# Kernel optimization log

Hardware: AMD Instinct MI355X
Metric: run time of the kernel (lower is better)

Reference implementation:

```python
import jax, jax.numpy as jnp
import numpy as np
from jax import lax

NALGOS = 64
NTASKS = 1024
LX_LEN = 512
TASK_DIFFICULTY_SCALE = 1.0


def setup_inputs() -> dict:
    key = jax.random.key(0)
    k1, k2, k3, k4, k5, k6 = jax.random.split(key, 6)
    lx = jax.random.randint(k1, (LX_LEN,), 0, NTASKS)
    # task similarity in [-1, 1] as in the original (np.random.random * 2 - 1)
    task_matrix = jax.random.uniform(k2, (NTASKS, NTASKS), dtype=jnp.float32) * 2.0 - 1.0
    # difficulty in (0, 1); offset slightly away from 0 for numerical sanity of result/difficulty
    task_difficulty = jax.random.uniform(k3, (NTASKS,), dtype=jnp.float32, minval=0.05, maxval=1.0)
    alg_efficiency = 0.5 + 0.02 * jax.random.normal(k4, (NALGOS,), dtype=jnp.float32)
    alg_memory = 0.5 + 0.10 * jax.random.normal(k5, (NALGOS,), dtype=jnp.float32)
    alg_experience_boost = 0.5 + 0.02 * jax.random.normal(k6, (NALGOS,), dtype=jnp.float32)
    return {
        "lx": lx,
        "task_matrix": task_matrix,
        "task_difficulty": task_difficulty,
        "alg_efficiency": alg_efficiency,
        "alg_memory": alg_memory,
        "alg_experience_boost": alg_experience_boost,
    }


def _performance(lx, task_matrix, task_difficulty, alg_efficiency, alg_memory, alg_experience_boost):
    nalgos = alg_efficiency.shape[0]
    ntasks = task_matrix.shape[0]
    dtype = task_matrix.dtype
    diff = task_difficulty * TASK_DIFFICULTY_SCALE  # [T]

    eff = alg_efficiency[:, None]          # [A,1]
    mem = alg_memory[:, None]              # [A,1]
    boost = alg_experience_boost[:, None]  # [A,1]

    def step(carry, task):
        result, sig = carry                 # each [A,T]
        row = task_matrix[task]             # [T] similarity of current lx task to every task2
        prior_perf = sig[:, task][:, None]  # [A,1] sig of current lx task at previous step
        result_next = result * mem + row[None, :] * (eff + prior_perf * boost)
        sig_next = jax.nn.sigmoid(result_next / diff[None, :]) * 2.0 - 1.0
        return (result_next, sig_next), sig_next

    init = (jnp.zeros((nalgos, ntasks), dtype), jnp.zeros((nalgos, ntasks), dtype))
    _, sig_steps = lax.scan(step, init, lx)  # [L,A,T]
    sig_steps = jnp.transpose(sig_steps, (1, 2, 0))  # [A,T,L]
    # prepend the zero initial step -> [A,T,L+1], matching torch output layout
    zero0 = jnp.zeros((nalgos, ntasks, 1), dtype)
    return jnp.concatenate([zero0, sig_steps], axis=-1)


def reference(lx, task_matrix, task_difficulty, alg_efficiency, alg_memory, alg_experience_boost):
    return _performance(lx, task_matrix, task_difficulty, alg_efficiency, alg_memory, alg_experience_boost)
```

## Files before the change

kernel.cpp:

```cpp
#include <hip/hip_runtime.h>

#define NALGOS 64
#define NTASKS 1024
#define LXLEN  512
#define TOUT   (LXLEN + 1)
#define PROWS  (LXLEN + 8)

__device__ __forceinline__ float rdlane(float v, int lane) {
    return __int_as_float(__builtin_amdgcn_readlane(__float_as_int(v), lane));
}

__global__ __launch_bounds__(256) void phase0_kernel(
    const int* __restrict__ lx, const float* __restrict__ tm,
    float* __restrict__ P)
{
    const int t = blockIdx.x;
    const int i = threadIdx.x;
    if (t < LXLEN) {
        const int row = lx[t] * NTASKS;
        P[t * LXLEN + i]       = tm[row + lx[i]];
        P[t * LXLEN + i + 256] = tm[row + lx[i + 256]];
    } else {
        P[t * LXLEN + i]       = 0.f;
        P[t * LXLEN + i + 256] = 0.f;
    }
}

__global__ __launch_bounds__(64) void phase1_kernel(
    const int*   __restrict__ lx,
    const float* __restrict__ P,
    const float* __restrict__ diff,
    const float* __restrict__ eff_g,
    const float* __restrict__ mem_g,
    const float* __restrict__ boost_g,
    float*       __restrict__ coef_out)
{
    const int a = blockIdx.x, lane = threadIdx.x;

    float nk[8]; float V[8];
    #pragma unroll
    for (int k = 0; k < 8; ++k) {
        const int tsk = lx[lane + 64 * k];
        nk[k] = -1.4426950408889634f / diff[tsk];
        V[k] = 0.f;
    }
    const float eff = eff_g[a], mem = mem_g[a], boost = boost_g[a];

    float G[8][8];
    #pragma unroll
    for (int d = 0; d < 8; ++d)
        #pragma unroll
        for (int k = 0; k < 8; ++k)
            G[d][k] = P[d * LXLEN + 64 * k + lane];

    float coef = eff;
    float* cout = coef_out + (size_t)a * LXLEN;

    #pragma unroll
    for (int q = 0; q < 8; ++q) {
        float cbuf = 0.f;
        for (int g = 0; g < 8; ++g) {
            const int tb = q * 64 + g * 8;
            #pragma unroll
            for (int j = 0; j < 8; ++j) {
                const float p = V[q] * nk[q];
                float x = rdlane(p, g * 8 + j);
                x = fminf(fmaxf(x, -126.f), 126.f);
                const float e = __builtin_exp2f(x);
                const float u = (1.f - e) * __builtin_amdgcn_rcpf(1.f + e);
                coef = __builtin_fmaf(u, boost, eff);
                cbuf = (lane == g * 8 + j) ? coef : cbuf;
                #pragma unroll
                for (int k = q; k < 8; ++k)
                    V[k] = __builtin_fmaf(V[k], mem, G[j][k] * coef);
                const float* rp = P + (tb + j + 8) * LXLEN + lane;
                #pragma unroll
                for (int k = q; k < 8; ++k)
                    G[j][k] = rp[64 * k];
            }
        }
        cout[q * 64 + lane] = cbuf;
    }
}

__global__ __launch_bounds__(256, 4) void phase2_kernel(
    const int*   __restrict__ lx,
    const float* __restrict__ tm,
    const float* __restrict__ diff,
    const float* __restrict__ mem_g,
    const float* __restrict__ coef,
    float*       __restrict__ out)
{
    const int b   = blockIdx.x;
    const int a   = b >> 5;
    const int c   = (b >> 2) & 7;
    const int seg = b & 3;
    const int tid = threadIdx.x;
    const int n   = (seg << 8) | tid;

    const int warm = (c >= 2) ? 128 : 64 * c;
    const int t0   = 64 * c - 1 - warm;

    __shared__ __align__(16) int   task_sh[224];
    __shared__ __align__(16) float coef_sh[224];
    __shared__ __align__(16) float ring[32 * 257];

    const int nfill = warm + 96;
    for (int i = tid; i < nfill; i += 256) {
        const int t = t0 + i;
        const bool ok = (t >= 0) && (t < LXLEN);
        task_sh[i] = ok ? lx[t] : 0;
        coef_sh[i] = ok ? coef[a * LXLEN + t] : 0.f;
    }

    const float mem   = mem_g[a];
    const float negkd = -1.4426950408889634f / diff[n];
    const int   d     = (16 - (n & 15)) & 15;
    float* rowp = out + ((size_t)a * NTASKS + n) * TOUT;
    float  r    = 0.f;
    float* ringc = ring + tid;

    const int wb = tid & 192;
    const int lq = tid & 15;
    const int qq = (tid >> 4) & 3;

    __syncthreads();

    float rbuf[16];
    #pragma unroll
    for (int j = 0; j < 16; ++j) {
        const int tk = __builtin_amdgcn_readfirstlane(task_sh[j]);
        rbuf[j] = tm[(size_t)tk * NTASKS + n];
    }

    for (int base = 0; base < warm; base += 16) {
        float nbuf[16];
        #pragma unroll
        for (int j = 0; j < 16; ++j) {
            const int tk = __builtin_amdgcn_readfirstlane(task_sh[base + 16 + j]);
            nbuf[j] = tm[(size_t)tk * NTASKS + n];
        }
        #pragma unroll
        for (int v = 0; v < 4; ++v) {
            const float4 cq = *(const float4*)&coef_sh[base + 4 * v];
            r = __builtin_fmaf(r, mem, rbuf[4 * v + 0] * cq.x);
            r = __builtin_fmaf(r, mem, rbuf[4 * v + 1] * cq.y);
            r = __builtin_fmaf(r, mem, rbuf[4 * v + 2] * cq.z);
            r = __builtin_fmaf(r, mem, rbuf[4 * v + 3] * cq.w);
        }
        #pragma unroll
        for (int j = 0; j < 16; ++j) rbuf[j] = nbuf[j];
    }

    #pragma unroll
    for (int rr = 0; rr < 5; ++rr) {
        const int base = warm + 16 * rr;
        float nbuf[16];
        #pragma unroll
        for (int j = 0; j < 16; ++j) {
            const int tk = __builtin_amdgcn_readfirstlane(task_sh[base + 16 + j]);
            nbuf[j] = tm[(size_t)tk * NTASKS + n];
        }
        #pragma unroll
        for (int v = 0; v < 4; ++v) {
            const float4 cq = *(const float4*)&coef_sh[base + 4 * v];
            const float cf[4] = { cq.x, cq.y, cq.z, cq.w };
            #pragma unroll
            for (int u4 = 0; u4 < 4; ++u4) {
                const int j = 4 * v + u4;
                r = __builtin_fmaf(r, mem, rbuf[j] * cf[u4]);
                float x = r * negkd;
                x = fminf(fmaxf(x, -126.f), 126.f);
                const float e = __builtin_exp2f(x);
                const float sig = (1.f - e) * __builtin_amdgcn_rcpf(1.f + e);
                ringc[((16 * rr + j - d) & 31) * 257] = sig;
                if (c == 0 && rr == 0 && j < d) rowp[j] = sig;
            }
        }
        if (rr >= 1) {
            const int g    = rr - 1;
            const int sb16 = (g & 1) << 4;
            #pragma unroll
            for (int sub = 0; sub < 16; ++sub) {
                const int tau = wb + 4 * sub + qq;
                const int nn  = (seg << 8) | tau;
                const int dd  = (16 - qq - 4 * (sub & 3)) & 15;
                const float vv = ring[(sb16 + lq) * 257 + tau];
                if (!(c == 7 && g == 3 && dd > 1)) {
                    out[((size_t)a * NTASKS + nn) * TOUT
                        + 64 * c + dd + 16 * g + lq] = vv;
                }
            }
        }
        #pragma unroll
        for (int j = 0; j < 16; ++j) rbuf[j] = nbuf[j];
    }

    if (c == 7) {
        const int tt0 = (d == 1) ? 513 : ((d == 0) ? 512 : 496 + d);
        #pragma unroll
        for (int u = 496; u <= 512; ++u) {
            if (u >= tt0) rowp[u] = ringc[(((u - 448) - d) & 31) * 257];
        }
    }
}

__global__ __launch_bounds__(1024) void fused_fallback_kernel(
    const int* __restrict__ lx, const float* __restrict__ tm,
    const float* __restrict__ diff, const float* __restrict__ eff_g,
    const float* __restrict__ mem_g, const float* __restrict__ boost_g,
    float* __restrict__ out)
{
    const int a = blockIdx.x, n = threadIdx.x;
    __shared__ int lx_sh[LXLEN];
    __shared__ float sbuf[2];
    if (n < LXLEN) lx_sh[n] = lx[n];
    if (n == 0) sbuf[0] = 0.0f;
    const float eff = eff_g[a], mem = mem_g[a], boost = boost_g[a];
    const float negkd = -1.4426950408889634f / diff[n];
    float* outp = out + ((size_t)a * NTASKS + n) * TOUT;
    outp[0] = 0.0f;
    float r = 0.0f;
    __syncthreads();
    for (int t = 0; t < LXLEN; ++t) {
        const int task = lx_sh[t];
        const float s = sbuf[t & 1];
        const float coef = __builtin_fmaf(s, boost, eff);
        const float row = tm[task * NTASKS + n];
        r = __builtin_fmaf(r, mem, row * coef);
        float x = r * negkd;
        x = fminf(fmaxf(x, -126.0f), 126.0f);
        const float e = __builtin_exp2f(x);
        const float sig = (1.0f - e) * __builtin_amdgcn_rcpf(1.0f + e);
        outp[t + 1] = sig;
        if (t + 1 < LXLEN && n == lx_sh[t + 1]) sbuf[(t + 1) & 1] = sig;
        __syncthreads();
    }
}

extern "C" void kernel_launch(void* const* d_in, const int* in_sizes, int n_in,
                              void* d_out, int out_size, void* d_ws, size_t ws_size,
                              hipStream_t stream) {
    const int*   lx    = (const int*)  d_in[0];
    const float* tm    = (const float*)d_in[1];
    const float* diff  = (const float*)d_in[2];
    const float* eff   = (const float*)d_in[3];
    const float* mem   = (const float*)d_in[4];
    const float* boost = (const float*)d_in[5];
    float* out = (float*)d_out;

    const size_t coef_elems = (size_t)NALGOS * LXLEN;
    const size_t P_elems    = (size_t)PROWS * LXLEN;
    const size_t need_bytes = (coef_elems + P_elems) * sizeof(float);

    if (ws_size >= need_bytes) {
        float* coef = (float*)d_ws;
        float* P    = coef + coef_elems;
        phase0_kernel<<<dim3(PROWS), dim3(256), 0, stream>>>(lx, tm, P);
        phase1_kernel<<<dim3(NALGOS), dim3(64), 0, stream>>>(
            lx, P, diff, eff, mem, boost, coef);
        phase2_kernel<<<dim3(NALGOS * 32), dim3(256), 0, stream>>>(
            lx, tm, diff, mem, coef, out);
    } else {
        fused_fallback_kernel<<<dim3(NALGOS), dim3(NTASKS), 0, stream>>>(
            lx, tm, diff, eff, mem, boost, out);
    }
}
```

Baseline: 225.9 us.

## Process eight algorithms per phase2 thread to reuse task_matrix loads

Phase2 blocks now handle 8 algorithms at once with 128-thread blocks, so each gathered task_matrix value is reused across 8 recurrences instead of being reloaded once per algorithm. The transpose ring buffer is reorganized per algorithm with a 16-row layout, and the tail write-out is folded into the main loop. Phase1 simplifies the sigmoid-to-coefficient formula into a single rcp plus fma and drops the exp clamp. The changes cut global gather traffic but raise register pressure and shrink the grid to 512 blocks, which may lower occupancy.

```diff
diff --git a/kernel.cpp b/kernel.cpp
--- a/kernel.cpp
+++ b/kernel.cpp
@@ -45,6 +45,7 @@
         V[k] = 0.f;
     }
     const float eff = eff_g[a], mem = mem_g[a], boost = boost_g[a];
+    const float twob = 2.f * boost, effmb = eff - boost;
 
     float G[8][8];
     #pragma unroll
@@ -64,11 +65,10 @@
             #pragma unroll
             for (int j = 0; j < 8; ++j) {
                 const float p = V[q] * nk[q];
-                float x = rdlane(p, g * 8 + j);
-                x = fminf(fmaxf(x, -126.f), 126.f);
+                const float x = rdlane(p, g * 8 + j);
                 const float e = __builtin_exp2f(x);
-                const float u = (1.f - e) * __builtin_amdgcn_rcpf(1.f + e);
-                coef = __builtin_fmaf(u, boost, eff);
+                const float w = __builtin_amdgcn_rcpf(1.f + e);
+                coef = __builtin_fmaf(twob, w, effmb);
                 cbuf = (lane == g * 8 + j) ? coef : cbuf;
                 #pragma unroll
                 for (int k = q; k < 8; ++k)
@@ -83,7 +83,7 @@
     }
 }
 
-__global__ __launch_bounds__(256, 4) void phase2_kernel(
+__global__ __launch_bounds__(128, 2) void phase2_kernel(
     const int*   __restrict__ lx,
     const float* __restrict__ tm,
     const float* __restrict__ diff,
@@ -92,35 +92,41 @@
     float*       __restrict__ out)
 {
     const int b   = blockIdx.x;
-    const int a   = b >> 5;
-    const int c   = (b >> 2) & 7;
-    const int seg = b & 3;
+    const int ag  = b >> 6;
+    const int c   = (b >> 3) & 7;
+    const int seg = b & 7;
     const int tid = threadIdx.x;
-    const int n   = (seg << 8) | tid;
-
-    const int warm = (c >= 2) ? 128 : 64 * c;
-    const int t0   = 64 * c - 1 - warm;
+    const int n   = (seg << 7) | tid;
+
+    const int warm  = (c >= 2) ? 128 : 64 * c;
+    const int t0    = 64 * c - 1 - warm;
+    const int nfill = warm + 96;
 
     __shared__ __align__(16) int   task_sh[224];
-    __shared__ __align__(16) float coef_sh[224];
-    __shared__ __align__(16) float ring[32 * 257];
-
-    const int nfill = warm + 96;
-    for (int i = tid; i < nfill; i += 256) {
+    __shared__ __align__(16) float coef_sh[8][224];
+    __shared__ __align__(16) float ring[8][16][129];
+
+    for (int i = tid; i < nfill; i += 128) {
         const int t = t0 + i;
         const bool ok = (t >= 0) && (t < LXLEN);
         task_sh[i] = ok ? lx[t] : 0;
-        coef_sh[i] = ok ? coef[a * LXLEN + t] : 0.f;
-    }
-
-    const float mem   = mem_g[a];
+        #pragma unroll
+        for (int g = 0; g < 8; ++g)
+            coef_sh[g][i] = ok ? coef[(ag * 8 + g) * LXLEN + t] : 0.f;
+    }
+
+    float memv[8];
+    #pragma unroll
+    for (int g = 0; g < 8; ++g) memv[g] = mem_g[ag * 8 + g];
+
     const float negkd = -1.4426950408889634f / diff[n];
     const int   d     = (16 - (n & 15)) & 15;
-    float* rowp = out + ((size_t)a * NTASKS + n) * TOUT;
-    float  r    = 0.f;
-    float* ringc = ring + tid;
-
-    const int wb = tid & 192;
+
+    float r[8];
+    #pragma unroll
+    for (int g = 0; g < 8; ++g) r[g] = 0.f;
+
+    const int wb = tid & 64;
     const int lq = tid & 15;
     const int qq = (tid >> 4) & 3;
 
@@ -142,17 +148,20 @@
         }
         #pragma unroll
         for (int v = 0; v < 4; ++v) {
-            const float4 cq = *(const float4*)&coef_sh[base + 4 * v];
-            r = __builtin_fmaf(r, mem, rbuf[4 * v + 0] * cq.x);
-            r = __builtin_fmaf(r, mem, rbuf[4 * v + 1] * cq.y);
-            r = __builtin_fmaf(r, mem, rbuf[4 * v + 2] * cq.z);
-            r = __builtin_fmaf(r, mem, rbuf[4 * v + 3] * cq.w);
+            #pragma unroll
+            for (int g = 0; g < 8; ++g) {
+                const float4 cq = *(const float4*)&coef_sh[g][base + 4 * v];
+                const float mg = memv[g];
+                r[g] = __builtin_fmaf(r[g], mg, rbuf[4 * v + 0] * cq.x);
+                r[g] = __builtin_fmaf(r[g], mg, rbuf[4 * v + 1] * cq.y);
+                r[g] = __builtin_fmaf(r[g], mg, rbuf[4 * v + 2] * cq.z);
+                r[g] = __builtin_fmaf(r[g], mg, rbuf[4 * v + 3] * cq.w);
+            }
         }
         #pragma unroll
         for (int j = 0; j < 16; ++j) rbuf[j] = nbuf[j];
     }
 
-    #pragma unroll
     for (int rr = 0; rr < 5; ++rr) {
         const int base = warm + 16 * rr;
         float nbuf[16];
@@ -162,46 +171,58 @@
             nbuf[j] = tm[(size_t)tk * NTASKS + n];
         }
         #pragma unroll
-        for (int v = 0; v < 4; ++v) {
-            const float4 cq = *(const float4*)&coef_sh[base + 4 * v];
-            const float cf[4] = { cq.x, cq.y, cq.z, cq.w };
-            #pragma unroll
-            for (int u4 = 0; u4 < 4; ++u4) {
-                const int j = 4 * v + u4;
-                r = __builtin_fmaf(r, mem, rbuf[j] * cf[u4]);
-                float x = r * negkd;
-                x = fminf(fmaxf(x, -126.f), 126.f);
-                const float e = __builtin_exp2f(x);
-                const float sig = (1.f - e) * __builtin_amdgcn_rcpf(1.f + e);
-                ringc[((16 * rr + j - d) & 31) * 257] = sig;
-                if (c == 0 && rr == 0 && j < d) rowp[j] = sig;
-            }
-        }
-        if (rr >= 1) {
-            const int g    = rr - 1;
-            const int sb16 = (g & 1) << 4;
-            #pragma unroll
-            for (int sub = 0; sub < 16; ++sub) {
-                const int tau = wb + 4 * sub + qq;
-                const int nn  = (seg << 8) | tau;
-                const int dd  = (16 - qq - 4 * (sub & 3)) & 15;
-                const float vv = ring[(sb16 + lq) * 257 + tau];
-                if (!(c == 7 && g == 3 && dd > 1)) {
-                    out[((size_t)a * NTASKS + nn) * TOUT
-                        + 64 * c + dd + 16 * g + lq] = vv;
+        for (int g = 0; g < 8; ++g) {
+            const float mg = memv[g];
+            float sb[16];
+            #pragma unroll
+            for (int v = 0; v < 4; ++v) {
+                const float4 cq = *(const float4*)&coef_sh[g][base + 4 * v];
+                const float cf[4] = { cq.x, cq.y, cq.z, cq.w };
+                #pragma unroll
+                for (int u4 = 0; u4 < 4; ++u4) {
+                    const int j = 4 * v + u4;
+                    r[g] = __builtin_fmaf(r[g], mg, rbuf[j] * cf[u4]);
+                    float x = r[g] * negkd;
+                    x = fminf(fmaxf(x, -126.f), 126.f);
+                    const float e = __builtin_exp2f(x);
+                    sb[j] = (1.f - e) * __builtin_amdgcn_rcpf(1.f + e);
                 }
             }
+            float* ringc = &ring[g][0][0] + tid;
+            #pragma unroll
+            for (int j = 0; j < 15; ++j)
+                if (j < d) ringc[(j + 16 - d) * 129] = sb[j];
+            if (rr >= 1) {
+                const int gr = rr - 1;
+                float* outg = out + (size_t)(ag * 8 + g) * NTASKS * TOUT;
+                #pragma unroll
+                for (int sub = 0; sub < 16; ++sub) {
+                    const int tau = wb + 4 * sub + qq;
+                    const int nn  = (seg << 7) | tau;
+                    const int dd  = (16 - (tau & 15)) & 15;
+                    const float vv = ring[g][lq][tau];
+                    if (!(c == 7 && gr == 3 && lq > 16 - dd))
+                        outg[(size_t)nn * TOUT + 64 * c + dd + 16 * gr + lq] = vv;
+                }
+            }
+            if (rr < 4) {
+                #pragma unroll
+                for (int j = 0; j < 16; ++j)
+                    if (j >= d) ringc[(j - d) * 129] = sb[j];
+            }
+            if (c == 0 && rr == 0) {
+                float* rowp = out + ((size_t)(ag * 8 + g) * NTASKS + n) * TOUT;
+                #pragma unroll
+                for (int j = 0; j < 15; ++j)
+                    if (j < d) rowp[j] = sb[j];
+            }
+            if (c == 7 && rr == 4 && d == 0) {
+                float* rowp = out + ((size_t)(ag * 8 + g) * NTASKS + n) * TOUT;
+                rowp[512] = sb[0];
+            }
         }
         #pragma unroll
         for (int j = 0; j < 16; ++j) rbuf[j] = nbuf[j];
-    }
-
-    if (c == 7) {
-        const int tt0 = (d == 1) ? 513 : ((d == 0) ? 512 : 496 + d);
-        #pragma unroll
-        for (int u = 496; u <= 512; ++u) {
-            if (u >= tt0) rowp[u] = ringc[(((u - 448) - d) & 31) * 257];
-        }
     }
 }
 
@@ -259,7 +280,7 @@
         phase0_kernel<<<dim3(PROWS), dim3(256), 0, stream>>>(lx, tm, P);
         phase1_kernel<<<dim3(NALGOS), dim3(64), 0, stream>>>(
             lx, P, diff, eff, mem, boost, coef);
-        phase2_kernel<<<dim3(NALGOS * 32), dim3(256), 0, stream>>>(
+        phase2_kernel<<<dim3(512), dim3(128), 0, stream>>>(
             lx, tm, diff, mem, coef, out);
     } else {
         fused_fallback_kernel<<<dim3(NALGOS), dim3(NTASKS), 0, stream>>>(
```

Measured after the change: 244.9 us. +8.4%, slower.
